# Kernel tuning notes

Hardware: AMD Instinct MI355X
Metric: run time of the kernel (lower is better)

Reference implementation:

```python
import jax, jax.numpy as jnp
import numpy as np

B, S, D = 512, 81, 1024
NH, DH = 16, 64
C, H1, G, FF = 32, 256, 256, 4096


def _ln(x, g, b, eps=1e-5):
    m = x.mean(-1, keepdims=True)
    v = ((x - m) ** 2).mean(-1, keepdims=True)
    return (x - m) * jax.lax.rsqrt(v + eps) * g + b


def _mish(x):
    return x * jnp.tanh(jax.nn.softplus(x))


def setup_inputs() -> dict:
    key = jax.random.key(0)
    ks = iter(jax.random.split(key, 32))
    n = lambda shape, s=0.02: jax.random.normal(next(ks), shape, jnp.float32) * s
    return {
        "x": jax.random.normal(next(ks), (B, S, D), jnp.float32),
        "w_compress": n((D, C)), "b_compress": jnp.zeros((C,)),
        "w_d1": n((S * C, H1)), "b_d1": jnp.zeros((H1,)),
        "ln1s_g": jnp.ones((H1,)), "ln1s_b": jnp.zeros((H1,)),
        "w_d2": n((H1, NH * G)), "b_d2": jnp.zeros((NH * G,)),
        "ln2s_g": jnp.ones((NH * G,)), "ln2s_b": jnp.zeros((NH * G,)),
        "w_gg": n((G, S * S)), "b_gg": jnp.zeros((S * S,)),
        "wq": n((D, D)), "bq": jnp.zeros((D,)),
        "wk": n((D, D)), "bk": jnp.zeros((D,)),
        "wv": n((D, D)), "bv": jnp.zeros((D,)),
        "wo": n((D, D)), "bo": jnp.zeros((D,)),
        "ln1_g": jnp.ones((D,)), "ln1_b": jnp.zeros((D,)),
        "w_f1": n((D, FF)), "b_f1": jnp.zeros((FF,)),
        "w_f2": n((FF, D)), "b_f2": jnp.zeros((D,)),
        "fln_g": jnp.ones((D,)), "fln_b": jnp.zeros((D,)),
    }


def reference(x, w_compress, b_compress, w_d1, b_d1, ln1s_g, ln1s_b,
              w_d2, b_d2, ln2s_g, ln2s_b, w_gg, b_gg,
              wq, bq, wk, bk, wv, bv, wo, bo, ln1_g, ln1_b,
              w_f1, b_f1, w_f2, b_f2, fln_g, fln_b):
    b = x.shape[0]
    # --- Smolgen: per-position attention bias ---
    h = jax.nn.silu(x @ w_compress + b_compress).reshape(b, S * C)
    h = jax.nn.silu(_ln(h @ w_d1 + b_d1, ln1s_g, ln1s_b))
    h = jax.nn.silu(_ln(h @ w_d2 + b_d2, ln2s_g, ln2s_b))
    h = h.reshape(b, NH, G)
    smol_bias = (h @ w_gg + b_gg).reshape(b, NH, S, S)
    # --- Attention with additive bias ---
    q = (x @ wq + bq).reshape(b, S, NH, DH)
    k = (x @ wk + bk).reshape(b, S, NH, DH)
    v = (x @ wv + bv).reshape(b, S, NH, DH)
    scores = jnp.einsum("bqhd,bkhd->bhqk", q, k) / np.sqrt(DH) + smol_bias
    attn = jax.nn.softmax(scores, axis=-1)
    out = jnp.einsum("bhqk,bkhd->bqhd", attn, v).reshape(b, S, D)
    h = _ln(out @ wo + bo + x, ln1_g, ln1_b)
    # --- FFN ---
    f = _mish(h @ w_f1 + b_f1)
    return _ln(f @ w_f2 + b_f2 + h, fln_g, fln_b)
```

## Files before the change

### kernel.cpp

```cpp
#include <hip/hip_runtime.h>
#include <hip/hip_bf16.h>
#include <cstdint>
#include <cstdio>

using bf16 = __hip_bfloat16;
typedef __attribute__((ext_vector_type(8))) short bf16x8;
typedef __attribute__((ext_vector_type(4))) float f32x4;

__device__ __forceinline__ void gload_lds16(const void* g, void* l) {
  __builtin_amdgcn_global_load_lds((__attribute__((address_space(1))) void*)g,
                                   (__attribute__((address_space(3))) void*)l,
                                   16, 0, 0);
}

__device__ __forceinline__ float bfu2f(unsigned short u) {
  return __uint_as_float((unsigned int)u << 16);
}
__device__ __forceinline__ unsigned short f2bfu(float f) {
  bf16 b = __float2bfloat16(f);
  return *(unsigned short*)&b;
}

enum { EP_NONE = 0, EP_SILU = 1, EP_MISH = 2, EP_RES = 3, EP_RESB = 4 };

template<int EPI>
__global__ __launch_bounds__(512, 2)
void gemm256(const bf16* __restrict__ A, const bf16* __restrict__ Bt,
             int N, int Nb, int K, int gy,
             const float* __restrict__ bias,
             const float* __restrict__ residf,
             const bf16* __restrict__ residb,
             bf16* __restrict__ outb)
{
  __shared__ char lds[131072];
  const int tid  = threadIdx.x;
  const int lane = tid & 63;
  const int wid  = tid >> 6;
  const int wm = wid >> 2, wn = wid & 3;
  const int lr = lane & 15, kg = lane >> 4;

  const int nwg = gridDim.x;
  const int q8 = nwg >> 3, r8 = nwg & 7;
  const int xcd = blockIdx.x & 7, idx = blockIdx.x >> 3;
  const int wg2 = (xcd < r8 ? xcd * (q8 + 1) : r8 * (q8 + 1) + (xcd - r8) * q8) + idx;
  const int by = wg2 % gy, bx = wg2 / gy;
  const long brow = (long)bx * 256, bcol = (long)by * 256;

  const size_t rb = (size_t)K * 2;
  const int r0   = wid * 8 + (lane >> 3);
  const int coff = ((lane & 7) ^ (lane >> 3)) << 4;
  const char* aS = (const char*)A  + (size_t)(brow + r0) * rb + coff;
  const char* bS = (const char*)Bt + (size_t)(bcol + r0) * rb + coff;
  char* ldsA = lds;
  char* ldsB = lds + 65536;
  const int luni = wid * 1024;

  const int ktiles = K >> 6;

  auto stage = [&](int t, int cur) {
    const size_t tb = (size_t)t * 128;
#pragma unroll
    for (int q = 0; q < 4; q++) {
      gload_lds16(aS + tb + (size_t)q * 64 * rb, ldsA + cur * 32768 + q * 8192 + luni);
      gload_lds16(bS + tb + (size_t)q * 64 * rb, ldsB + cur * 32768 + q * 8192 + luni);
    }
  };

  f32x4 acc[8][4] = {};

  stage(0, 0);
  stage(1, 1);

  const int swz   = (lr & 7) << 4;
  const int abase = (wm * 128 + lr) * 128;
  const int bbase = (wn * 64 + lr) * 128;

  for (int t = 0; t < ktiles; ++t) {
    const int cur = t & 1;
    if (t + 1 < ktiles) asm volatile("s_waitcnt vmcnt(8)" ::: "memory");
    else                asm volatile("s_waitcnt vmcnt(0)" ::: "memory");
    __builtin_amdgcn_s_barrier();
    const char* pA = ldsA + cur * 32768;
    const char* pB = ldsB + cur * 32768;
#pragma unroll
    for (int ks = 0; ks < 2; ks++) {
      const int kb = ((((ks << 2) + kg) << 4)) ^ swz;
      bf16x8 a[8], b[4];
#pragma unroll
      for (int i = 0; i < 8; i++) a[i] = *(const bf16x8*)(pA + abase + i * 2048 + kb);
#pragma unroll
      for (int j = 0; j < 4; j++) b[j] = *(const bf16x8*)(pB + bbase + j * 2048 + kb);
      __builtin_amdgcn_s_setprio(1);
#pragma unroll
      for (int i = 0; i < 8; i++)
#pragma unroll
        for (int j = 0; j < 4; j++)
          acc[i][j] = __builtin_amdgcn_mfma_f32_16x16x32_bf16(a[i], b[j], acc[i][j], 0, 0, 0);
      __builtin_amdgcn_s_setprio(0);
    }
    __builtin_amdgcn_s_barrier();
    if (t + 2 < ktiles) stage(t + 2, cur);
  }

  char* lC = lds;
  const int cr = kg * 4;
#pragma unroll
  for (int j = 0; j < 4; j++) {
    const int tcol = wn * 64 + j * 16 + lr;
    const long gcol = bcol + tcol;
    const float bv = (gcol < Nb) ? bias[gcol] : 0.f;
#pragma unroll
    for (int i = 0; i < 8; i++) {
#pragma unroll
      for (int r = 0; r < 4; r++) {
        const int row = wm * 128 + i * 16 + cr + r;
        float v = acc[i][j][r] + bv;
        if constexpr (EPI == EP_MISH) {
          float e = __expf(fminf(v, 20.f));
          float u = (1.f + e); u *= u;
          v = v * (u - 1.f) / (u + 1.f);
        }
        *(unsigned short*)(lC + row * 512 + ((tcol * 2) ^ ((row & 12) << 3))) = f2bfu(v);
      }
    }
  }
  __syncthreads();
  const int trow = tid >> 5;
  const int tcb  = (tid & 31) * 16;
#pragma unroll
  for (int it = 0; it < 16; ++it) {
    const int row = it * 16 + trow;
    bf16x8 vv = *(const bf16x8*)(lC + row * 512 + (tcb ^ ((row & 12) << 3)));
    const long grow = brow + row;
    bf16* dst = outb + grow * (long)N + bcol + (tcb >> 1);
    if constexpr (EPI == EP_RES) {
      const float* rs = residf + grow * (long)N + bcol + (tcb >> 1);
      float4 ra = *(const float4*)rs, rb2 = *(const float4*)(rs + 4);
      float rv[8] = {ra.x, ra.y, ra.z, ra.w, rb2.x, rb2.y, rb2.z, rb2.w};
      bf16x8 ov;
#pragma unroll
      for (int e = 0; e < 8; e++)
        ov[e] = (short)f2bfu(bfu2f((unsigned short)vv[e]) + rv[e]);
      *(bf16x8*)dst = ov;
    } else if constexpr (EPI == EP_RESB) {
      bf16x8 rb3 = *(const bf16x8*)(residb + grow * (long)N + bcol + (tcb >> 1));
      bf16x8 ov;
#pragma unroll
      for (int e = 0; e < 8; e++)
        ov[e] = (short)f2bfu(bfu2f((unsigned short)vv[e]) + bfu2f((unsigned short)rb3[e]));
      *(bf16x8*)dst = ov;
    } else {
      *(bf16x8*)dst = vv;
    }
  }
}

template<int EPI, bool OUTF>
__global__ __launch_bounds__(256)
void gemm_kernel(const bf16* __restrict__ A, const bf16* __restrict__ Bt,
                 int M, int N, int K,
                 const float* __restrict__ bias,
                 const float* __restrict__ residf,
                 const bf16* __restrict__ residb,
                 float* __restrict__ outf, bf16* __restrict__ outb)
{
  __shared__ bf16 lA[128 * 32];
  __shared__ bf16 lB[128 * 32];
  const int tid  = threadIdx.x;
  const int lane = tid & 63;
  const int wvid = tid >> 6;
  const int wr = (wvid >> 1) * 64;
  const int wc = (wvid & 1) * 64;
  const long brow = (long)blockIdx.x * 128;
  const long bcol = (long)blockIdx.y * 128;
  const int lr = lane & 15;
  const int k8 = (lane >> 4) * 8;

  const int lofs0 = wvid * 1024;
  const int lofs1 = lofs0 + 4096;
  const int o0 = lofs0 + lane * 16;
  const int o1 = o0 + 4096;
  const int r0 = o0 >> 6, c0 = o0 & 63;
  const int r1 = o1 >> 6, c1 = o1 & 63;

  f32x4 acc[4][4] = {};

  for (int k0 = 0; k0 < K; k0 += 32) {
    const long kb = (long)k0 * 2;
    gload_lds16((const char*)A  + ((brow + r0) * (long)K) * 2 + kb + c0, (char*)lA + lofs0);
    gload_lds16((const char*)A  + ((brow + r1) * (long)K) * 2 + kb + c1, (char*)lA + lofs1);
    gload_lds16((const char*)Bt + ((bcol + r0) * (long)K) * 2 + kb + c0, (char*)lB + lofs0);
    gload_lds16((const char*)Bt + ((bcol + r1) * (long)K) * 2 + kb + c1, (char*)lB + lofs1);
    __syncthreads();
    bf16x8 af[4], bf_[4];
#pragma unroll
    for (int i = 0; i < 4; i++)
      af[i] = *(const bf16x8*)&lA[(wr + i * 16 + lr) * 32 + k8];
#pragma unroll
    for (int j = 0; j < 4; j++)
      bf_[j] = *(const bf16x8*)&lB[(wc + j * 16 + lr) * 32 + k8];
#pragma unroll
    for (int i = 0; i < 4; i++)
#pragma unroll
      for (int j = 0; j < 4; j++)
        acc[i][j] = __builtin_amdgcn_mfma_f32_16x16x32_bf16(af[i], bf_[j], acc[i][j], 0, 0, 0);
    __syncthreads();
  }

  const int cr = (lane >> 4) * 4;
  const int cc = lane & 15;
#pragma unroll
  for (int j = 0; j < 4; j++) {
    const long col = bcol + wc + j * 16 + cc;
    if (col >= N) continue;
    const float bv = bias[col];
#pragma unroll
    for (int i = 0; i < 4; i++) {
#pragma unroll
      for (int r = 0; r < 4; r++) {
        const long row = brow + wr + i * 16 + cr + r;
        float v = acc[i][j][r] + bv;
        if constexpr (EPI == EP_RES)  v += residf[row * N + col];
        if constexpr (EPI == EP_RESB) v += __bfloat162float(residb[row * N + col]);
        if constexpr (EPI == EP_SILU) v = v / (1.f + __expf(-v));
        if constexpr (EPI == EP_MISH) {
          float t = __expf(fminf(v, 20.f));
          float u = (1.f + t); u *= u;
          v = v * (u - 1.f) / (u + 1.f);
        }
        if constexpr (OUTF) outf[row * N + col] = v;
        else                outb[row * N + col] = __float2bfloat16(v);
      }
    }
  }
}

__global__ __launch_bounds__(256)
void transpose_to_bf16(const float* __restrict__ W, bf16* __restrict__ Bt,
                       int K, int N, int Npad)
{
  __shared__ float tile[32][33];
  const int n0 = blockIdx.x * 32, k0 = blockIdx.y * 32;
  const int tx = threadIdx.x, ty = threadIdx.y;
  for (int r = ty; r < 32; r += 8) {
    int k = k0 + r, n = n0 + tx;
    tile[r][tx] = (k < K && n < N) ? W[(size_t)k * N + n] : 0.f;
  }
  __syncthreads();
  for (int r = ty; r < 32; r += 8) {
    int n = n0 + r, k = k0 + tx;
    if (n < Npad && k < K) Bt[(size_t)n * K + k] = __float2bfloat16(tile[tx][r]);
  }
}

__global__ __launch_bounds__(256)
void cvt_f32_bf16(const float* __restrict__ in, bf16* __restrict__ out, long n)
{
  long i = ((long)blockIdx.x * 256 + threadIdx.x) * 4;
  const long stride = (long)gridDim.x * 256 * 4;
  for (; i < n; i += stride) {
    float4 v = *(const float4*)(in + i);
    out[i]     = __float2bfloat16(v.x);
    out[i + 1] = __float2bfloat16(v.y);
    out[i + 2] = __float2bfloat16(v.z);
    out[i + 3] = __float2bfloat16(v.w);
  }
}

__global__ __launch_bounds__(256)
void pack3(const float* __restrict__ a, const float* __restrict__ b,
           const float* __restrict__ c, float* __restrict__ o, int n)
{
  int i = blockIdx.x * 256 + threadIdx.x;
  if (i < n) { o[i] = a[i]; o[n + i] = b[i]; o[2 * n + i] = c[i]; }
}

template<int ACT>
__global__ __launch_bounds__(256)
void ln_rows(const float* __restrict__ inf, const float* __restrict__ g,
             const float* __restrict__ be, bf16* __restrict__ ob, int C)
{
  const long row = blockIdx.x;
  float s = 0.f, ss = 0.f;
  for (int c = threadIdx.x; c < C; c += 256) {
    float v = inf[row * C + c];
    s += v; ss += v * v;
  }
#pragma unroll
  for (int o = 32; o; o >>= 1) { s += __shfl_xor(s, o); ss += __shfl_xor(ss, o); }
  __shared__ float p1[4], p2[4];
  const int wv = threadIdx.x >> 6;
  if ((threadIdx.x & 63) == 0) { p1[wv] = s; p2[wv] = ss; }
  __syncthreads();
  s  = p1[0] + p1[1] + p1[2] + p1[3];
  ss = p2[0] + p2[1] + p2[2] + p2[3];
  const float mean = s / C;
  const float var  = ss / C - mean * mean;
  const float rstd = rsqrtf(var + 1e-5f);
  for (int c = threadIdx.x; c < C; c += 256) {
    float v = (inf[row * C + c] - mean) * rstd * g[c] + be[c];
    if (ACT == 1) v = v / (1.f + __expf(-v));
    ob[row * C + c] = __float2bfloat16(v);
  }
}

template<bool WF, bool WB>
__global__ __launch_bounds__(256)
void ln1024(const bf16* __restrict__ inb, const float* __restrict__ g,
            const float* __restrict__ be, float* __restrict__ of,
            bf16* __restrict__ ob)
{
  const size_t row = blockIdx.x;
  const int t = threadIdx.x;
  const unsigned short* xr = (const unsigned short*)(inb + row * 1024) + t * 4;
  ushort4 raw = *(const ushort4*)xr;
  float v0 = bfu2f(raw.x), v1 = bfu2f(raw.y), v2 = bfu2f(raw.z), v3 = bfu2f(raw.w);
  float s = v0 + v1 + v2 + v3;
  float ss = v0 * v0 + v1 * v1 + v2 * v2 + v3 * v3;
#pragma unroll
  for (int o = 32; o; o >>= 1) { s += __shfl_xor(s, o); ss += __shfl_xor(ss, o); }
  __shared__ float p1[4], p2[4];
  const int wv = t >> 6;
  if ((t & 63) == 0) { p1[wv] = s; p2[wv] = ss; }
  __syncthreads();
  s  = p1[0] + p1[1] + p1[2] + p1[3];
  ss = p2[0] + p2[1] + p2[2] + p2[3];
  const float mean = s * (1.f / 1024.f);
  const float var  = ss * (1.f / 1024.f) - mean * mean;
  const float rstd = rsqrtf(var + 1e-5f);
  const int c = t * 4;
  float4 gg = *(const float4*)(g + c);
  float4 bb = *(const float4*)(be + c);
  float y0 = (v0 - mean) * rstd * gg.x + bb.x;
  float y1 = (v1 - mean) * rstd * gg.y + bb.y;
  float y2 = (v2 - mean) * rstd * gg.z + bb.z;
  float y3 = (v3 - mean) * rstd * gg.w + bb.w;
  if (WF) *(float4*)(of + row * 1024 + c) = make_float4(y0, y1, y2, y3);
  if (WB) {
    ushort4 o4 = { f2bfu(y0), f2bfu(y1), f2bfu(y2), f2bfu(y3) };
    *(ushort4*)((unsigned short*)(ob + row * 1024) + t * 4) = o4;
  }
}

__global__ __launch_bounds__(384)
void attn_mfma(const bf16* __restrict__ qkv, const bf16* __restrict__ smol,
               bf16* __restrict__ out)
{
  __shared__ char smem[37888];
  char* lqc = smem;
  char* lkc = smem + 12288;
  short* lvt = (short*)(smem + 24576);
  char* lpc = smem;

  const int b = blockIdx.x, h = blockIdx.y;
  const int tid = threadIdx.x;
  const int lane = tid & 63;
  const int w = tid >> 6;
  const int lr = lane & 15;
  const int kg = lane >> 4;

  const size_t qkv_base = (size_t)(b * 81) * 3072 + h * 64;

  for (int idx = tid; idx < 1296; idx += 384) {
    int which = idx >= 648;
    int e = which ? idx - 648 : idx;
    int s = e >> 3, c = e & 7;
    bf16x8 v = *(const bf16x8*)(qkv + qkv_base + (size_t)s * 3072 + which * 1024 + c * 8);
    char* base = which ? lkc : lqc;
    *(bf16x8*)(base + s * 128 + ((c ^ (s & 7)) << 4)) = v;
  }
  for (int idx = tid; idx < 648; idx += 384) {
    int s = idx >> 3, c = idx & 7;
    bf16x8 v = *(const bf16x8*)(qkv + qkv_base + (size_t)s * 3072 + 2048 + c * 8);
#pragma unroll
    for (int j = 0; j < 8; j++) lvt[(c * 8 + j) * 104 + s] = v[j];
  }
  {
    bf16x8 z = {};
    for (int idx = tid; idx < 240; idx += 384) {
      int which = idx >= 120;
      int e = which ? idx - 120 : idx;
      int s = 81 + (e >> 3), c = e & 7;
      char* base = which ? lkc : lqc;
      *(bf16x8*)(base + s * 128 + ((c ^ (s & 7)) << 4)) = z;
    }
    for (int idx = tid; idx < 1472; idx += 384) {
      int d = idx / 23, s = 81 + idx % 23;
      lvt[d * 104 + s] = 0;
    }
  }
  __syncthreads();

  f32x4 sacc[6] = {};
  const int m = w * 16 + lr;
#pragma unroll
  for (int ks = 0; ks < 2; ks++) {
    bf16x8 af = *(const bf16x8*)(lqc + m * 128 + ((((ks << 2) + kg) ^ (m & 7)) << 4));
#pragma unroll
    for (int j = 0; j < 6; j++) {
      int n = j * 16 + lr;
      bf16x8 bf_ = *(const bf16x8*)(lkc + n * 128 + ((((ks << 2) + kg) ^ (n & 7)) << 4));
      sacc[j] = __builtin_amdgcn_mfma_f32_16x16x32_bf16(af, bf_, sacc[j], 0, 0, 0);
    }
  }

  const bf16* smrow = smol + (size_t)(b * 16 + h) * 6656;
  float p[6][4];
#pragma unroll
  for (int j = 0; j < 6; j++) {
    int col = j * 16 + lr;
#pragma unroll
    for (int r = 0; r < 4; r++) {
      int row = w * 16 + kg * 4 + r;
      float sv = sacc[j][r] * 0.125f;
      if (col < 81) {
        if (row < 81) sv += __bfloat162float(smrow[row * 81 + col]);
      } else sv = -3.0e38f;
      p[j][r] = sv;
    }
  }
#pragma unroll
  for (int r = 0; r < 4; r++) {
    float mx = p[0][r];
#pragma unroll
    for (int j = 1; j < 6; j++) mx = fmaxf(mx, p[j][r]);
    mx = fmaxf(mx, __shfl_xor(mx, 1)); mx = fmaxf(mx, __shfl_xor(mx, 2));
    mx = fmaxf(mx, __shfl_xor(mx, 4)); mx = fmaxf(mx, __shfl_xor(mx, 8));
    float sum = 0.f;
#pragma unroll
    for (int j = 0; j < 6; j++) { float e = __expf(p[j][r] - mx); p[j][r] = e; sum += e; }
    sum += __shfl_xor(sum, 1); sum += __shfl_xor(sum, 2);
    sum += __shfl_xor(sum, 4); sum += __shfl_xor(sum, 8);
    float inv = 1.f / sum;
#pragma unroll
    for (int j = 0; j < 6; j++) p[j][r] *= inv;
  }
  __syncthreads();

#pragma unroll
  for (int j = 0; j < 6; j++) {
    int col = j * 16 + lr;
#pragma unroll
    for (int r = 0; r < 4; r++) {
      int row = w * 16 + kg * 4 + r;
      *(unsigned short*)(lpc + row * 256 + ((((col >> 3) ^ (row & 7)) << 4)) + (col & 7) * 2)
          = f2bfu(p[j][r]);
    }
  }
  __syncthreads();

  f32x4 oacc[4] = {};
#pragma unroll
  for (int ks = 0; ks < 3; ks++) {
    bf16x8 pa = *(const bf16x8*)(lpc + m * 256 + ((((ks << 2) + kg) ^ (m & 7)) << 4));
#pragma unroll
    for (int j2 = 0; j2 < 4; j2++) {
      int n = j2 * 16 + lr;
      bf16x8 vb = *(const bf16x8*)((char*)lvt + n * 208 + ((ks << 2) + kg) * 16);
      oacc[j2] = __builtin_amdgcn_mfma_f32_16x16x32_bf16(pa, vb, oacc[j2], 0, 0, 0);
    }
  }
#pragma unroll
  for (int j2 = 0; j2 < 4; j2++) {
    int d = j2 * 16 + lr;
#pragma unroll
    for (int r = 0; r < 4; r++) {
      int row = w * 16 + kg * 4 + r;
      if (row < 81)
        out[(size_t)(b * 81 + row) * 1024 + h * 64 + d] = __float2bfloat16(oacc[j2][r]);
    }
  }
}

extern "C" void kernel_launch(void* const* d_in, const int* in_sizes, int n_in,
                              void* d_out, int out_size, void* d_ws, size_t ws_size,
                              hipStream_t stream)
{
  const float* x     = (const float*)d_in[0];
  const float* w_c   = (const float*)d_in[1];
  const float* b_c   = (const float*)d_in[2];
  const float* w_d1  = (const float*)d_in[3];
  const float* b_d1  = (const float*)d_in[4];
  const float* ln1sg = (const float*)d_in[5];
  const float* ln1sb = (const float*)d_in[6];
  const float* w_d2  = (const float*)d_in[7];
  const float* b_d2  = (const float*)d_in[8];
  const float* ln2sg = (const float*)d_in[9];
  const float* ln2sb = (const float*)d_in[10];
  const float* w_gg  = (const float*)d_in[11];
  const float* b_gg  = (const float*)d_in[12];
  const float* wq    = (const float*)d_in[13];
  const float* bq    = (const float*)d_in[14];
  const float* wk    = (const float*)d_in[15];
  const float* bk    = (const float*)d_in[16];
  const float* wvp   = (const float*)d_in[17];
  const float* bv    = (const float*)d_in[18];
  const float* wo    = (const float*)d_in[19];
  const float* bo    = (const float*)d_in[20];
  const float* ln1g  = (const float*)d_in[21];
  const float* ln1b  = (const float*)d_in[22];
  const float* w_f1  = (const float*)d_in[23];
  const float* b_f1  = (const float*)d_in[24];
  const float* w_f2  = (const float*)d_in[25];
  const float* b_f2  = (const float*)d_in[26];
  const float* flng  = (const float*)d_in[27];
  const float* flnb  = (const float*)d_in[28];
  float* out = (float*)d_out;

  char* ws = (char*)d_ws;
  size_t off = 0;
  auto alloc = [&](size_t bytes) -> char* {
    char* p = ws + off; off += (bytes + 255) & ~(size_t)255; return p;
  };
  bf16*  Bt_c  = (bf16*)alloc(262144);
  bf16*  Bt_d1 = (bf16*)alloc(1327104);
  bf16*  Bt_d2 = (bf16*)alloc(2097152);
  bf16*  Bt_gg = (bf16*)alloc(3407872);
  bf16*  Bt_qkv= (bf16*)alloc(6291456);
  bf16*  Bt_wo = (bf16*)alloc(2097152);
  bf16*  Bt_f1 = (bf16*)alloc(8388608);
  bf16*  Bt_f2 = (bf16*)alloc(8388608);
  float* bqkv  = (float*)alloc(12288);
  bf16*  h0b   = (bf16*)alloc(2654208);
  float* pre_s = (float*)alloc(8388608);
  bf16*  h1b   = (bf16*)alloc(262144);
  bf16*  h2b   = (bf16*)alloc(4194304);
  char*  S1    = alloc(84934656);
  char*  S2    = alloc(339738624);
  char*  S3    = alloc(109051904);

  bf16* xb     = (bf16*)S1;
  bf16* aob    = (bf16*)S1;
  bf16* hmidb  = (bf16*)S1;
  bf16* qkvb   = (bf16*)S2;
  bf16* fb     = (bf16*)S2;
  bf16* smol   = (bf16*)S3;
  bf16* preln1 = (bf16*)S3;
  bf16* preln2 = (bf16*)S3;

  if (ws_size < off) { printf("WS too small: %zu < %zu\n", ws_size, off); return; }

  const dim3 tb(32, 8);
  transpose_to_bf16<<<dim3(4, 32),   tb, 0, stream>>>(w_c,  Bt_c,  1024, 32,   128);
  transpose_to_bf16<<<dim3(8, 81),   tb, 0, stream>>>(w_d1, Bt_d1, 2592, 256,  256);
  transpose_to_bf16<<<dim3(128, 8),  tb, 0, stream>>>(w_d2, Bt_d2, 256,  4096, 4096);
  transpose_to_bf16<<<dim3(208, 8),  tb, 0, stream>>>(w_gg, Bt_gg, 256,  6561, 6656);
  transpose_to_bf16<<<dim3(32, 32),  tb, 0, stream>>>(wq,   Bt_qkv,             1024, 1024, 1024);
  transpose_to_bf16<<<dim3(32, 32),  tb, 0, stream>>>(wk,   Bt_qkv + 1024*1024, 1024, 1024, 1024);
  transpose_to_bf16<<<dim3(32, 32),  tb, 0, stream>>>(wvp,  Bt_qkv + 2048*1024, 1024, 1024, 1024);
  transpose_to_bf16<<<dim3(32, 32),  tb, 0, stream>>>(wo,   Bt_wo, 1024, 1024, 1024);
  transpose_to_bf16<<<dim3(128, 32), tb, 0, stream>>>(w_f1, Bt_f1, 1024, 4096, 4096);
  transpose_to_bf16<<<dim3(32, 128), tb, 0, stream>>>(w_f2, Bt_f2, 4096, 1024, 1024);
  pack3<<<4, 256, 0, stream>>>(bq, bk, bv, bqkv, 1024);
  cvt_f32_bf16<<<2048, 256, 0, stream>>>(x, xb, 42467328L);

  gemm_kernel<EP_SILU, false><<<dim3(324, 1), 256, 0, stream>>>(
      xb, Bt_c, 41472, 32, 1024, b_c, nullptr, nullptr, nullptr, h0b);
  gemm_kernel<EP_NONE, true><<<dim3(4, 2), 256, 0, stream>>>(
      h0b, Bt_d1, 512, 256, 2592, b_d1, nullptr, nullptr, pre_s, nullptr);
  ln_rows<1><<<512, 256, 0, stream>>>(pre_s, ln1sg, ln1sb, h1b, 256);
  gemm_kernel<EP_NONE, true><<<dim3(4, 32), 256, 0, stream>>>(
      h1b, Bt_d2, 512, 4096, 256, b_d2, nullptr, nullptr, pre_s, nullptr);
  ln_rows<1><<<512, 256, 0, stream>>>(pre_s, ln2sg, ln2sb, h2b, 4096);
  gemm256<EP_NONE><<<32 * 26, 512, 0, stream>>>(
      h2b, Bt_gg, 6656, 6561, 256, 26, b_gg, nullptr, nullptr, smol);

  gemm256<EP_NONE><<<162 * 12, 512, 0, stream>>>(
      xb, Bt_qkv, 3072, 3072, 1024, 12, bqkv, nullptr, nullptr, qkvb);
  attn_mfma<<<dim3(512, 16), 384, 0, stream>>>(qkvb, smol, aob);
  gemm256<EP_RES><<<162 * 4, 512, 0, stream>>>(
      aob, Bt_wo, 1024, 1024, 1024, 4, bo, x, nullptr, preln1);
  ln1024<false, true><<<41472, 256, 0, stream>>>(preln1, ln1g, ln1b, nullptr, hmidb);

  gemm256<EP_MISH><<<162 * 16, 512, 0, stream>>>(
      hmidb, Bt_f1, 4096, 4096, 1024, 16, b_f1, nullptr, nullptr, fb);
  gemm256<EP_RESB><<<162 * 4, 512, 0, stream>>>(
      fb, Bt_f2, 1024, 1024, 4096, 4, b_f2, nullptr, hmidb, preln2);
  ln1024<true, false><<<41472, 256, 0, stream>>>(preln2, flng, flnb, out, nullptr);
}
```

Measured before the change: 1.960 ms.

## Restructure 256x256 GEMM into quadrant-phased pipeline with interleaved half-tile loads

Rewrites the gemm256 main loop so each warp computes four 64x32 quadrants in phases. Each phase reads only half of the A or B fragments from LDS and issues the next tile's global-to-LDS loads in 128-row halves between MFMA bursts, which is meant to overlap loads with compute and cut register pressure from fragment arrays. Launch bounds drop to one block per CU to free registers. The wo projection now takes its residual from the bf16 copy of x rather than fp32 x, which halves residual read traffic but lowers residual precision. The attention output is moved to a separate buffer so xb stays valid for that residual read.

```diff
diff --git a/kernel.cpp b/kernel.cpp
--- a/kernel.cpp
+++ b/kernel.cpp
@@ -24,7 +24,7 @@
 enum { EP_NONE = 0, EP_SILU = 1, EP_MISH = 2, EP_RES = 3, EP_RESB = 4 };
 
 template<int EPI>
-__global__ __launch_bounds__(512, 2)
+__global__ __launch_bounds__(512, 1)
 void gemm256(const bf16* __restrict__ A, const bf16* __restrict__ Bt,
              int N, int Nb, int K, int gy,
              const float* __restrict__ bias,
@@ -43,84 +43,117 @@
   const int q8 = nwg >> 3, r8 = nwg & 7;
   const int xcd = blockIdx.x & 7, idx = blockIdx.x >> 3;
   const int wg2 = (xcd < r8 ? xcd * (q8 + 1) : r8 * (q8 + 1) + (xcd - r8) * q8) + idx;
-  const int by = wg2 % gy, bx = wg2 / gy;
+  const int bx = wg2 / gy, by = wg2 % gy;
   const long brow = (long)bx * 256, bcol = (long)by * 256;
 
   const size_t rb = (size_t)K * 2;
-  const int r0   = wid * 8 + (lane >> 3);
-  const int coff = ((lane & 7) ^ (lane >> 3)) << 4;
-  const char* aS = (const char*)A  + (size_t)(brow + r0) * rb + coff;
-  const char* bS = (const char*)Bt + (size_t)(bcol + r0) * rb + coff;
+  const int srow8 = wid * 8 + (lane >> 3);
+  const int coff  = ((lane & 7) ^ (lane >> 3)) << 4;
+  const char* aS = (const char*)A  + (size_t)(brow + srow8) * rb + coff;
+  const char* bS = (const char*)Bt + (size_t)(bcol + srow8) * rb + coff;
   char* ldsA = lds;
   char* ldsB = lds + 65536;
   const int luni = wid * 1024;
 
-  const int ktiles = K >> 6;
-
-  auto stage = [&](int t, int cur) {
-    const size_t tb = (size_t)t * 128;
-#pragma unroll
-    for (int q = 0; q < 4; q++) {
-      gload_lds16(aS + tb + (size_t)q * 64 * rb, ldsA + cur * 32768 + q * 8192 + luni);
-      gload_lds16(bS + tb + (size_t)q * 64 * rb, ldsB + cur * 32768 + q * 8192 + luni);
-    }
+  const int kt = K >> 6;
+
+  auto stA = [&](int t, int h) {
+    const char* s = aS + (size_t)(h * 128) * rb + (size_t)t * 128;
+    char* d = ldsA + (t & 1) * 32768 + h * 16384 + luni;
+    gload_lds16(s, d);
+    gload_lds16(s + (size_t)64 * rb, d + 8192);
   };
-
-  f32x4 acc[8][4] = {};
-
-  stage(0, 0);
-  stage(1, 1);
-
-  const int swz   = (lr & 7) << 4;
-  const int abase = (wm * 128 + lr) * 128;
-  const int bbase = (wn * 64 + lr) * 128;
-
-  for (int t = 0; t < ktiles; ++t) {
-    const int cur = t & 1;
-    if (t + 1 < ktiles) asm volatile("s_waitcnt vmcnt(8)" ::: "memory");
-    else                asm volatile("s_waitcnt vmcnt(0)" ::: "memory");
+  auto stB = [&](int t, int h) {
+    const char* s = bS + (size_t)(h * 128) * rb + (size_t)t * 128;
+    char* d = ldsB + (t & 1) * 32768 + h * 16384 + luni;
+    gload_lds16(s, d);
+    gload_lds16(s + (size_t)64 * rb, d + 8192);
+  };
+
+  f32x4 acc[4][4][2] = {};
+  bf16x8 afr[4][2], bfr[2][2];
+
+  stA(0, 0); stB(0, 0); stB(0, 1); stA(0, 1);
+  stA(1, 0); stB(1, 1); stA(1, 1);
+
+  const int swz  = lr & 7;
+  const int arow = wm * 64 + lr;
+  const int brw  = wn * 32 + lr;
+
+#define KCH(ks) ((((((ks) << 2) + kg) ^ swz)) << 4)
+#define RD_A(rh) \
+  _Pragma("unroll") for (int i = 0; i < 4; i++) \
+  _Pragma("unroll") for (int ks = 0; ks < 2; ks++) \
+    afr[i][ks] = *(const bf16x8*)(pA + (rh) * 16384 + (arow + i * 16) * 128 + KCH(ks));
+#define RD_B(ch) \
+  _Pragma("unroll") for (int j = 0; j < 2; j++) \
+  _Pragma("unroll") for (int ks = 0; ks < 2; ks++) \
+    bfr[j][ks] = *(const bf16x8*)(pB + (ch) * 16384 + (brw + j * 16) * 128 + KCH(ks));
+#define MFMA_Q(q) \
+  asm volatile("s_waitcnt lgkmcnt(0)" ::: "memory"); \
+  __builtin_amdgcn_sched_barrier(0); \
+  __builtin_amdgcn_s_setprio(1); \
+  _Pragma("unroll") for (int i = 0; i < 4; i++) \
+  _Pragma("unroll") for (int j = 0; j < 2; j++) \
+  _Pragma("unroll") for (int ks = 0; ks < 2; ks++) \
+    acc[q][i][j] = __builtin_amdgcn_mfma_f32_16x16x32_bf16(afr[i][ks], bfr[j][ks], acc[q][i][j], 0, 0, 0); \
+  __builtin_amdgcn_s_setprio(0);
+
+  for (int t = 0; t < kt; ++t) {
+    const char* pA = ldsA + (t & 1) * 32768;
+    const char* pB = ldsB + (t & 1) * 32768;
+
+    if (t + 1 < kt) asm volatile("s_waitcnt vmcnt(6)" ::: "memory");
+    else            asm volatile("s_waitcnt vmcnt(0)" ::: "memory");
     __builtin_amdgcn_s_barrier();
-    const char* pA = ldsA + cur * 32768;
-    const char* pB = ldsB + cur * 32768;
-#pragma unroll
-    for (int ks = 0; ks < 2; ks++) {
-      const int kb = ((((ks << 2) + kg) << 4)) ^ swz;
-      bf16x8 a[8], b[4];
-#pragma unroll
-      for (int i = 0; i < 8; i++) a[i] = *(const bf16x8*)(pA + abase + i * 2048 + kb);
-#pragma unroll
-      for (int j = 0; j < 4; j++) b[j] = *(const bf16x8*)(pB + bbase + j * 2048 + kb);
-      __builtin_amdgcn_s_setprio(1);
-#pragma unroll
-      for (int i = 0; i < 8; i++)
-#pragma unroll
-        for (int j = 0; j < 4; j++)
-          acc[i][j] = __builtin_amdgcn_mfma_f32_16x16x32_bf16(a[i], b[j], acc[i][j], 0, 0, 0);
-      __builtin_amdgcn_s_setprio(0);
-    }
+    RD_A(0) RD_B(0)
+    if (t + 1 < kt) stB(t + 1, 0);
+    MFMA_Q(0)
+
     __builtin_amdgcn_s_barrier();
-    if (t + 2 < ktiles) stage(t + 2, cur);
-  }
+    RD_B(1)
+    if (t + 2 < kt) stA(t + 2, 0);
+    MFMA_Q(1)
+
+    __builtin_amdgcn_s_barrier();
+    RD_A(1)
+    if (t + 2 < kt) stB(t + 2, 1);
+    MFMA_Q(2)
+
+    __builtin_amdgcn_s_barrier();
+    RD_B(0)
+    if (t + 2 < kt) stA(t + 2, 1);
+    MFMA_Q(3)
+  }
+#undef KCH
+#undef RD_A
+#undef RD_B
+#undef MFMA_Q
+
+  __syncthreads();
 
   char* lC = lds;
-  const int cr = kg * 4;
-#pragma unroll
-  for (int j = 0; j < 4; j++) {
-    const int tcol = wn * 64 + j * 16 + lr;
-    const long gcol = bcol + tcol;
-    const float bv = (gcol < Nb) ? bias[gcol] : 0.f;
-#pragma unroll
-    for (int i = 0; i < 8; i++) {
-#pragma unroll
-      for (int r = 0; r < 4; r++) {
-        const int row = wm * 128 + i * 16 + cr + r;
-        float v = acc[i][j][r] + bv;
-        if constexpr (EPI == EP_MISH) {
-          float e = __expf(fminf(v, 20.f));
-          float u = (1.f + e); u *= u;
-          v = v * (u - 1.f) / (u + 1.f);
+#pragma unroll
+  for (int q = 0; q < 4; q++) {
+    const int rh = (q >= 2), ch = (q == 1 || q == 2);
+#pragma unroll
+    for (int j = 0; j < 2; j++) {
+      const int tcol = ch * 128 + wn * 32 + j * 16 + lr;
+      const long gcol = bcol + tcol;
+      const float bv = (gcol < Nb) ? bias[gcol] : 0.f;
+#pragma unroll
+      for (int i = 0; i < 4; i++) {
+#pragma unroll
+        for (int r = 0; r < 4; r++) {
+          const int row = rh * 128 + wm * 64 + i * 16 + kg * 4 + r;
+          float v = acc[q][i][j][r] + bv;
+          if constexpr (EPI == EP_MISH) {
+            float e = __expf(fminf(v, 20.f));
+            float u = (1.f + e); u *= u;
+            v = v * (u - 1.f) / (u + 1.f);
+          }
+          *(unsigned short*)(lC + row * 512 + ((tcol * 2) ^ ((row & 12) << 3))) = f2bfu(v);
         }
-        *(unsigned short*)(lC + row * 512 + ((tcol * 2) ^ ((row & 12) << 3))) = f2bfu(v);
       }
     }
   }
@@ -530,9 +563,9 @@
   char*  S3    = alloc(109051904);
 
   bf16* xb     = (bf16*)S1;
-  bf16* aob    = (bf16*)S1;
   bf16* hmidb  = (bf16*)S1;
   bf16* qkvb   = (bf16*)S2;
+  bf16* aob    = (bf16*)(S2 + 254803968);
   bf16* fb     = (bf16*)S2;
   bf16* smol   = (bf16*)S3;
   bf16* preln1 = (bf16*)S3;
@@ -568,8 +601,8 @@
   gemm256<EP_NONE><<<162 * 12, 512, 0, stream>>>(
       xb, Bt_qkv, 3072, 3072, 1024, 12, bqkv, nullptr, nullptr, qkvb);
   attn_mfma<<<dim3(512, 16), 384, 0, stream>>>(qkvb, smol, aob);
-  gemm256<EP_RES><<<162 * 4, 512, 0, stream>>>(
-      aob, Bt_wo, 1024, 1024, 1024, 4, bo, x, nullptr, preln1);
+  gemm256<EP_RESB><<<162 * 4, 512, 0, stream>>>(
+      aob, Bt_wo, 1024, 1024, 1024, 4, bo, nullptr, xb, preln1);
   ln1024<false, true><<<41472, 256, 0, stream>>>(preln1, ln1g, ln1b, nullptr, hmidb);
 
   gemm256<EP_MISH><<<162 * 16, 512, 0, stream>>>(
```

Result: faster. 1.705 ms (-13.0%).
